# Kernel optimization log

Hardware: AMD Instinct MI355X
Metric: run time of the kernel (lower is better)

The kernel has to match this reference:

```python
import jax, jax.numpy as jnp
import numpy as np

N, E = 50000, 800000
IN_DIM, HEADS, OUT_DIM = 128, 4, 32
NEG_SLOPE = 0.2
EPS = 1e-16


def setup_inputs() -> dict:
    key = jax.random.key(0)
    k = jax.random.split(key, 6)
    x = jax.random.normal(k[0], (N, IN_DIM), dtype=jnp.float32)
    edge_index = jax.random.randint(k[1], (2, E), 0, N, dtype=jnp.int64)
    # xavier-uniform-ish params
    lim_w = float(np.sqrt(6.0 / (IN_DIM + HEADS * OUT_DIM)))
    W = jax.random.uniform(k[2], (HEADS * OUT_DIM, IN_DIM), minval=-lim_w, maxval=lim_w, dtype=jnp.float32)
    lim_a = float(np.sqrt(6.0 / (1 + HEADS * OUT_DIM)))
    att_src = jax.random.uniform(k[3], (1, HEADS, OUT_DIM), minval=-lim_a, maxval=lim_a, dtype=jnp.float32)
    att_dst = jax.random.uniform(k[4], (1, HEADS, OUT_DIM), minval=-lim_a, maxval=lim_a, dtype=jnp.float32)
    bias = jnp.zeros((HEADS * OUT_DIM,), dtype=jnp.float32)
    return {"x": x, "edge_index": edge_index, "W": W, "att_src": att_src, "att_dst": att_dst, "bias": bias}


def reference(x, edge_index, W, att_src, att_dst, bias):
    n = x.shape[0]
    h = (x @ W.T).reshape(n, HEADS, OUT_DIM)           # (N,H,D)
    src, dst = edge_index[0], edge_index[1]
    a_src = jnp.sum(h * att_src, axis=-1)              # (N,H)
    a_dst = jnp.sum(h * att_dst, axis=-1)              # (N,H)
    alpha = a_src[src] + a_dst[dst]                    # (E,H)
    alpha = jax.nn.leaky_relu(alpha, NEG_SLOPE)
    # segment (per-dst) softmax over edges, per head
    m = jax.ops.segment_max(alpha, dst, num_segments=n)   # (N,H)
    ex = jnp.exp(alpha - m[dst])
    s = jax.ops.segment_sum(ex, dst, num_segments=n)      # (N,H)
    alpha = ex / (s[dst] + EPS)                            # (E,H)
    # dropout p=0 (eval) -> identity
    msg = h[src] * alpha[..., None]                        # (E,H,D)
    out = jax.ops.segment_sum(msg, dst, num_segments=n)    # (N,H,D)
    out = out.reshape(n, HEADS * OUT_DIM) + bias
    alpha_pooled = alpha.mean(axis=-1)                     # (E,)
    return out, alpha_pooled
```

## Files before the change

kernel.cpp:

```cpp
#include <hip/hip_runtime.h>

#define NNODES 50000
#define NEDGES 800000
#define HD 128
#define NEG 0.2f
#define MTILE 64
#define LDW 136
#define MAXD 64
#define GEMMB ((NNODES + MTILE - 1) / MTILE)
#define NBINS 196
#define CAP 5120
#define ABLK ((NEDGES + 2047) / 2048)

typedef __attribute__((ext_vector_type(8))) short short8;
typedef __attribute__((ext_vector_type(4))) float floatx4;

static __device__ inline unsigned short f2bf(float f) {
    unsigned u = __float_as_uint(f);
    return (unsigned short)((u + 0x7FFF + ((u >> 16) & 1)) >> 16);
}
static __device__ inline float bf2f(unsigned short u) {
    return __uint_as_float(((unsigned)u) << 16);
}
static __device__ inline float lrelu_exp(float a) {
    a = (a > 0.f) ? a : NEG * a;
    return __expf(a);
}

__global__ __launch_bounds__(256, 4) void gat_main(
    const float* __restrict__ x, const float* __restrict__ W,
    const float* __restrict__ att_src, const float* __restrict__ att_dst,
    const int* __restrict__ ei,
    unsigned short* __restrict__ h, float* __restrict__ asrc,
    float* __restrict__ adst, int* __restrict__ Sg, int* __restrict__ sbuf)
{
    __shared__ __align__(16) unsigned short Wl[128 * LDW];
    const int t = threadIdx.x;

    if (blockIdx.x >= GEMMB) {
        int* hist = (int*)Wl;
        int* sh   = hist + 256;
        int* run  = sh + 256;
        int* lbuf = run + 256;
        const int blk = blockIdx.x - GEMMB;
        const int e0 = blk * 2048 + t * 8;
        const bool act = (e0 < NEDGES);
        const int cnt = (blk == ABLK - 1) ? (NEDGES - blk * 2048) : 2048;
        int4 s0 = make_int4(0, 0, 0, 0), s1 = s0, d0 = s0, d1 = s0;
        if (act) {
            s0 = *(const int4*)(ei + e0);
            s1 = *(const int4*)(ei + e0 + 4);
            d0 = *(const int4*)(ei + NEDGES + e0);
            d1 = *(const int4*)(ei + NEDGES + e0 + 4);
        }
        hist[t] = 0;
        __syncthreads();
        if (act) {
            atomicAdd(&hist[d0.x >> 8], 1); atomicAdd(&hist[d0.y >> 8], 1);
            atomicAdd(&hist[d0.z >> 8], 1); atomicAdd(&hist[d0.w >> 8], 1);
            atomicAdd(&hist[d1.x >> 8], 1); atomicAdd(&hist[d1.y >> 8], 1);
            atomicAdd(&hist[d1.z >> 8], 1); atomicAdd(&hist[d1.w >> 8], 1);
        }
        __syncthreads();
        int hv = hist[t];
        sh[t] = hv;
        __syncthreads();
        for (int off = 1; off < 256; off <<= 1) {
            int u = (t >= off) ? sh[t - off] : 0;
            __syncthreads();
            sh[t] += u;
            __syncthreads();
        }
        int ex = sh[t] - hv;
        run[t] = ex;
        Sg[blk * 257 + t] = ex;
        if (t == 0) Sg[blk * 257 + 256] = cnt;
        __syncthreads();
        if (act) {
            int ss[8] = {s0.x, s0.y, s0.z, s0.w, s1.x, s1.y, s1.z, s1.w};
            int dd[8] = {d0.x, d0.y, d0.z, d0.w, d1.x, d1.y, d1.z, d1.w};
#pragma unroll
            for (int j = 0; j < 8; j++) {
                int slot = atomicAdd(&run[dd[j] >> 8], 1);
                lbuf[slot] = ((dd[j] & 255) << 16) | ss[j];
            }
        }
        __syncthreads();
        for (int i = t; i < cnt; i += 256)
            sbuf[blk * 2048 + i] = lbuf[i];
        return;
    }

    const int rowBase = blockIdx.x * MTILE;

    for (int idx = t * 8; idx < 128 * 128; idx += 2048) {
        int r = idx >> 7, c = idx & 127;
        float4 v0 = *(const float4*)(W + idx);
        float4 v1 = *(const float4*)(W + idx + 4);
        short8 u;
        u[0] = (short)f2bf(v0.x); u[1] = (short)f2bf(v0.y);
        u[2] = (short)f2bf(v0.z); u[3] = (short)f2bf(v0.w);
        u[4] = (short)f2bf(v1.x); u[5] = (short)f2bf(v1.y);
        u[6] = (short)f2bf(v1.z); u[7] = (short)f2bf(v1.w);
        *(short8*)(Wl + r * LDW + c) = u;
    }

    const int wave = t >> 6;
    const int lane = t & 63;
    const int c16  = lane & 15;
    const int quad = lane >> 4;
    const int xr   = rowBase + wave * 16 + c16;
    short8 av[4];
#pragma unroll
    for (int kc = 0; kc < 4; kc++) {
        float4 v0 = make_float4(0.f, 0.f, 0.f, 0.f);
        float4 v1 = v0;
        if (xr < NNODES) {
            const float* p = x + (size_t)xr * 128 + kc * 32 + quad * 8;
            v0 = *(const float4*)p;
            v1 = *(const float4*)(p + 4);
        }
        short8 u;
        u[0] = (short)f2bf(v0.x); u[1] = (short)f2bf(v0.y);
        u[2] = (short)f2bf(v0.z); u[3] = (short)f2bf(v0.w);
        u[4] = (short)f2bf(v1.x); u[5] = (short)f2bf(v1.y);
        u[6] = (short)f2bf(v1.z); u[7] = (short)f2bf(v1.w);
        av[kc] = u;
    }
    __syncthreads();

    floatx4 acc[8];
#pragma unroll
    for (int nt = 0; nt < 8; nt++) acc[nt] = (floatx4)(0.f);

#pragma unroll
    for (int kc = 0; kc < 4; kc++) {
#pragma unroll
        for (int nt = 0; nt < 8; nt++) {
            short8 bv = *(const short8*)(Wl + (nt * 16 + c16) * LDW + kc * 32 + quad * 8);
            acc[nt] = __builtin_amdgcn_mfma_f32_16x16x32_bf16(av[kc], bv, acc[nt], 0, 0, 0);
        }
    }

    float As[8], Ad[8];
#pragma unroll
    for (int nt = 0; nt < 8; nt++) {
        As[nt] = att_src[nt * 16 + c16];
        Ad[nt] = att_dst[nt * 16 + c16];
    }
#pragma unroll
    for (int r = 0; r < 4; r++) {
        const int gr = rowBase + wave * 16 + quad * 4 + r;
#pragma unroll
        for (int hh = 0; hh < 4; hh++) {
            float ps = acc[2 * hh][r] * As[2 * hh] + acc[2 * hh + 1][r] * As[2 * hh + 1];
            float pd = acc[2 * hh][r] * Ad[2 * hh] + acc[2 * hh + 1][r] * Ad[2 * hh + 1];
#pragma unroll
            for (int m = 8; m >= 1; m >>= 1) {
                ps += __shfl_xor(ps, m, 64);
                pd += __shfl_xor(pd, m, 64);
            }
            if (c16 == 0 && gr < NNODES) {
                asrc[gr * 4 + hh] = ps;
                adst[gr * 4 + hh] = pd;
            }
        }
    }

    __syncthreads();
#pragma unroll
    for (int r = 0; r < 4; r++) {
        const int lr = wave * 16 + quad * 4 + r;
#pragma unroll
        for (int nt = 0; nt < 8; nt++)
            Wl[lr * LDW + nt * 16 + c16] = f2bf(acc[nt][r]);
    }
    __syncthreads();
    for (int idx = t * 8; idx < MTILE * 128; idx += 2048) {
        int r = idx >> 7, c = idx & 127;
        int g = rowBase + r;
        if (g < NNODES)
            *(short8*)(h + (size_t)g * HD + c) = *(const short8*)(Wl + r * LDW + c);
    }
}

__global__ __launch_bounds__(1024) void gat_bin(
    const int* __restrict__ Sg, const int* __restrict__ sbuf,
    const float* __restrict__ asrc, const float* __restrict__ adst,
    int* __restrict__ coffB, int* __restrict__ coffE,
    unsigned short* __restrict__ csr, float* __restrict__ rsumr)
{
    __shared__ int s0arr[391];
    __shared__ int segoff[391];
    __shared__ int ebi[CAP];
    __shared__ unsigned short ebs[CAP];
    __shared__ int hist[256], run[256], sh[512];
    const int t = threadIdx.x;
    const int b = blockIdx.x;

    int s0v = 0, lenv = 0;
    if (t < 391) {
        s0v = Sg[t * 257 + b];
        lenv = Sg[t * 257 + b + 1] - s0v;
        s0arr[t] = s0v;
    }
    if (t < 256) hist[t] = 0;
    if (t < 512) sh[t] = (t < 391) ? lenv : 0;
    __syncthreads();
    for (int off = 1; off < 512; off <<= 1) {
        int u = (t < 512 && t >= off) ? sh[t - off] : 0;
        __syncthreads();
        if (t < 512) sh[t] += u;
        __syncthreads();
    }
    if (t < 391) segoff[t] = sh[t] - lenv;
    __syncthreads();
    const int c_b = sh[390];

    for (int i = t; i < c_b; i += 1024) {
        int lo = 0, hi = 390;
        while (lo < hi) {
            int mid = (lo + hi + 1) >> 1;
            if (segoff[mid] <= i) lo = mid; else hi = mid - 1;
        }
        int e = sbuf[lo * 2048 + s0arr[lo] + (i - segoff[lo])];
        ebi[i] = e;
        atomicAdd(&hist[(e >> 16) & 255], 1);
    }
    __syncthreads();

    int hv = (t < 256) ? hist[t] : 0;
    int ex = 0;
    if (t < 256) sh[t] = hv;
    __syncthreads();
    for (int off = 1; off < 256; off <<= 1) {
        int u = (t < 256 && t >= off) ? sh[t - off] : 0;
        __syncthreads();
        if (t < 256) sh[t] += u;
        __syncthreads();
    }
    if (t < 256) {
        ex = sh[t] - hv;
        run[t] = ex;
        int n = b * 256 + t;
        if (n < NNODES) {
            coffB[n] = b * CAP + ex;
            coffE[n] = b * CAP + ex + hv;
        }
    }
    __syncthreads();

    for (int i = t; i < c_b; i += 1024) {
        int e = ebi[i];
        int slot = atomicAdd(&run[(e >> 16) & 255], 1);
        ebs[slot] = (unsigned short)(e & 0xFFFF);
    }
    __syncthreads();

    for (int i = t; i < c_b; i += 1024)
        csr[(size_t)b * CAP + i] = ebs[i];

    if (t < 256) {
        int n = b * 256 + t;
        if (n < NNODES) {
            const float4 bn = *(const float4*)(adst + n * 4);
            float4 s4 = make_float4(0.f, 0.f, 0.f, 0.f);
            for (int i = ex; i < ex + hv; i++) {
                int s = ebs[i];
                float4 a = *(const float4*)(asrc + s * 4);
                s4.x += lrelu_exp(a.x + bn.x);
                s4.y += lrelu_exp(a.y + bn.y);
                s4.z += lrelu_exp(a.z + bn.z);
                s4.w += lrelu_exp(a.w + bn.w);
            }
            float4 r4;
            r4.x = 1.f / (s4.x + 1e-16f);
            r4.y = 1.f / (s4.y + 1e-16f);
            r4.z = 1.f / (s4.z + 1e-16f);
            r4.w = 1.f / (s4.w + 1e-16f);
            *(float4*)(rsumr + n * 4) = r4;
        }
    }
}

__global__ __launch_bounds__(256) void gat_node(
    const int* __restrict__ coffB, const int* __restrict__ coffE,
    const unsigned short* __restrict__ csr,
    const float* __restrict__ asrc, const float* __restrict__ adst,
    const unsigned short* __restrict__ h, const float* __restrict__ bias,
    float* __restrict__ out, const float* __restrict__ rsumr)
{
    __shared__ unsigned short sh_src[4 * MAXD];
    __shared__ float sh_w[4 * MAXD * 4];
    const int t = threadIdx.x;
    const int w = t >> 6;
    const int lane = t & 63;
    const int n = blockIdx.x * 4 + w;
    const int beg = coffB[n], end = coffE[n];
    const int deg = end - beg;
    const int lim = (deg < MAXD) ? deg : MAXD;
    const int base = w * MAXD;

    const float4 rs4 = *(const float4*)(rsumr + n * 4);

    if (lane < lim) {
        int s = csr[beg + lane];
        const float4 bn = *(const float4*)(adst + n * 4);
        float4 a = *(const float4*)(asrc + s * 4);
        float4 wv;
        wv.x = lrelu_exp(a.x + bn.x);
        wv.y = lrelu_exp(a.y + bn.y);
        wv.z = lrelu_exp(a.z + bn.z);
        wv.w = lrelu_exp(a.w + bn.w);
        sh_src[base + lane] = (unsigned short)s;
        *(float4*)(sh_w + (base + lane) * 4) = wv;
    }

    const int quad = lane >> 4;
    const int i16  = lane & 15;
    const int head = i16 >> 2;
    const float rsel = (head == 0) ? rs4.x : (head == 1) ? rs4.y
                      : (head == 2) ? rs4.z : rs4.w;

    float accA[8], accB[8];
#pragma unroll
    for (int m = 0; m < 8; m++) { accA[m] = 0.f; accB[m] = 0.f; }

    int j = 0;
    for (; j + 16 <= lim; j += 16) {
        int e0 = j + quad, e1 = j + 4 + quad, e2 = j + 8 + quad, e3 = j + 12 + quad;
        int s0 = sh_src[base + e0];
        int s1 = sh_src[base + e1];
        int s2 = sh_src[base + e2];
        int s3 = sh_src[base + e3];
        float w0 = sh_w[(base + e0) * 4 + head] * rsel;
        float w1 = sh_w[(base + e1) * 4 + head] * rsel;
        float w2 = sh_w[(base + e2) * 4 + head] * rsel;
        float w3 = sh_w[(base + e3) * 4 + head] * rsel;
        short8 u0 = *(const short8*)(h + (size_t)s0 * HD + i16 * 8);
        short8 u1 = *(const short8*)(h + (size_t)s1 * HD + i16 * 8);
        short8 u2 = *(const short8*)(h + (size_t)s2 * HD + i16 * 8);
        short8 u3 = *(const short8*)(h + (size_t)s3 * HD + i16 * 8);
#pragma unroll
        for (int m = 0; m < 8; m++) {
            accA[m] = fmaf(bf2f((unsigned short)u0[m]), w0, accA[m]);
            accB[m] = fmaf(bf2f((unsigned short)u1[m]), w1, accB[m]);
            accA[m] = fmaf(bf2f((unsigned short)u2[m]), w2, accA[m]);
            accB[m] = fmaf(bf2f((unsigned short)u3[m]), w3, accB[m]);
        }
    }
    for (; j + 4 <= lim; j += 4) {
        int e0 = j + quad;
        int s0 = sh_src[base + e0];
        float w0 = sh_w[(base + e0) * 4 + head] * rsel;
        short8 u0 = *(const short8*)(h + (size_t)s0 * HD + i16 * 8);
#pragma unroll
        for (int m = 0; m < 8; m++)
            accA[m] = fmaf(bf2f((unsigned short)u0[m]), w0, accA[m]);
    }
    if (quad < lim - j) {
        int s0 = sh_src[base + j + quad];
        float w0 = sh_w[(base + j + quad) * 4 + head] * rsel;
        short8 u0 = *(const short8*)(h + (size_t)s0 * HD + i16 * 8);
#pragma unroll
        for (int m = 0; m < 8; m++)
            accA[m] = fmaf(bf2f((unsigned short)u0[m]), w0, accA[m]);
    }
    if (deg > MAXD) {
        const float4 bn = *(const float4*)(adst + n * 4);
        const float bnh = (head == 0) ? bn.x : (head == 1) ? bn.y
                         : (head == 2) ? bn.z : bn.w;
        for (int jj = beg + MAXD + quad; jj < end; jj += 4) {
            int s0 = csr[jj];
            float w0 = lrelu_exp(asrc[s0 * 4 + head] + bnh) * rsel;
            short8 u0 = *(const short8*)(h + (size_t)s0 * HD + i16 * 8);
#pragma unroll
            for (int m = 0; m < 8; m++)
                accA[m] = fmaf(bf2f((unsigned short)u0[m]), w0, accA[m]);
        }
    }

#pragma unroll
    for (int m = 0; m < 8; m++) {
        accA[m] += accB[m];
        accA[m] += __shfl_xor(accA[m], 16, 64);
        accA[m] += __shfl_xor(accA[m], 32, 64);
    }
    if (quad < 2) {
        const float4 b4 = *(const float4*)(bias + i16 * 8 + quad * 4);
        float4 st;
        if (quad == 0) {
            st.x = accA[0] + b4.x; st.y = accA[1] + b4.y;
            st.z = accA[2] + b4.z; st.w = accA[3] + b4.w;
        } else {
            st.x = accA[4] + b4.x; st.y = accA[5] + b4.y;
            st.z = accA[6] + b4.z; st.w = accA[7] + b4.w;
        }
        *(float4*)(out + (size_t)n * HD + i16 * 8 + quad * 4) = st;
    }
}

static __device__ inline float apool1(
    int s, int d, const float* __restrict__ asrc,
    const float* __restrict__ adst, const float* __restrict__ rsumr)
{
    float4 a = *(const float4*)(asrc + s * 4);
    float4 b = *(const float4*)(adst + d * 4);
    float4 r = *(const float4*)(rsumr + d * 4);
    return 0.25f * (lrelu_exp(a.x + b.x) * r.x + lrelu_exp(a.y + b.y) * r.y +
                    lrelu_exp(a.z + b.z) * r.z + lrelu_exp(a.w + b.w) * r.w);
}

__global__ __launch_bounds__(256) void gat_apool(
    const int* __restrict__ ei, const float* __restrict__ asrc,
    const float* __restrict__ adst, const float* __restrict__ rsumr,
    float* __restrict__ apool)
{
    int e0 = (blockIdx.x * 256 + threadIdx.x) * 4;
    if (e0 >= NEDGES) return;
    int4 s = *(const int4*)(ei + e0);
    int4 d = *(const int4*)(ei + NEDGES + e0);
    float4 r;
    r.x = apool1(s.x, d.x, asrc, adst, rsumr);
    r.y = apool1(s.y, d.y, asrc, adst, rsumr);
    r.z = apool1(s.z, d.z, asrc, adst, rsumr);
    r.w = apool1(s.w, d.w, asrc, adst, rsumr);
    *(float4*)(apool + e0) = r;
}

extern "C" void kernel_launch(void* const* d_in, const int* in_sizes, int n_in,
                              void* d_out, int out_size, void* d_ws, size_t ws_size,
                              hipStream_t stream)
{
    const float* x       = (const float*)d_in[0];
    const int*   ei      = (const int*)d_in[1];
    const float* W       = (const float*)d_in[2];
    const float* att_src = (const float*)d_in[3];
    const float* att_dst = (const float*)d_in[4];
    const float* bias    = (const float*)d_in[5];

    float* out   = (float*)d_out;
    float* apool = out + (size_t)NNODES * HD;

    unsigned short* h = (unsigned short*)d_ws;
    float* asrc  = (float*)(h + (size_t)NNODES * HD);
    float* adst  = asrc + NNODES * 4;
    float* rsumr = adst + NNODES * 4;
    int*   Sg    = (int*)(rsumr + NNODES * 4);
    int*   coffB = Sg + ABLK * 257 + 4;
    int*   coffE = coffB + NNODES + 4;
    int*   sbuf  = coffE + NNODES + 4;
    unsigned short* csr = (unsigned short*)(sbuf + (size_t)ABLK * 2048);

    gat_main<<<GEMMB + ABLK, 256, 0, stream>>>(
        x, W, att_src, att_dst, ei, h, asrc, adst, Sg, sbuf);
    gat_bin<<<NBINS, 1024, 0, stream>>>(
        Sg, sbuf, asrc, adst, coffB, coffE, csr, rsumr);
    gat_node<<<NNODES / 4, 256, 0, stream>>>(
        coffB, coffE, csr, asrc, adst, h, bias, out, rsumr);
    gat_apool<<<(NEDGES / 4 + 255) / 256, 256, 0, stream>>>(
        ei, asrc, adst, rsumr, apool);
}
```

Baseline: 166.5 us.

## Parallelize softmax denominators with LDS atomics and fuse apool into node kernel

The per-destination exp-sum in the binning kernel is computed by all 1024 threads, each handling edges with shared-memory float atomics, instead of one thread per node looping serially over its edges. The edge-pooling kernel is merged into the node aggregation kernel as extra leading blocks, removing a launch and allowing overlap. The node kernel also gets a higher occupancy hint. This trades the serial loop's load imbalance for LDS atomic contention and nondeterministic summation order.

Result: slower. 172.4 us (+3.5%).

```diff
diff --git a/kernel.cpp b/kernel.cpp
--- a/kernel.cpp
+++ b/kernel.cpp
@@ -11,6 +11,7 @@
 #define NBINS 196
 #define CAP 5120
 #define ABLK ((NEDGES + 2047) / 2048)
+#define APOOLB ((NEDGES / 4 + 255) / 256)
 
 typedef __attribute__((ext_vector_type(8))) short short8;
 typedef __attribute__((ext_vector_type(4))) float floatx4;
@@ -195,6 +196,7 @@
     __shared__ int ebi[CAP];
     __shared__ unsigned short ebs[CAP];
     __shared__ int hist[256], run[256], sh[512];
+    __shared__ float sum4[256 * 4];
     const int t = threadIdx.x;
     const int b = blockIdx.x;
 
@@ -205,6 +207,7 @@
         s0arr[t] = s0v;
     }
     if (t < 256) hist[t] = 0;
+    sum4[t] = 0.f;
     if (t < 512) sh[t] = (t < 391) ? lenv : 0;
     __syncthreads();
     for (int off = 1; off < 512; off <<= 1) {
@@ -230,7 +233,6 @@
     __syncthreads();
 
     int hv = (t < 256) ? hist[t] : 0;
-    int ex = 0;
     if (t < 256) sh[t] = hv;
     __syncthreads();
     for (int off = 1; off < 256; off <<= 1) {
@@ -240,7 +242,7 @@
         __syncthreads();
     }
     if (t < 256) {
-        ex = sh[t] - hv;
+        int ex = sh[t] - hv;
         run[t] = ex;
         int n = b * 256 + t;
         if (n < NNODES) {
@@ -259,43 +261,72 @@
 
     for (int i = t; i < c_b; i += 1024)
         csr[(size_t)b * CAP + i] = ebs[i];
+    for (int i = t; i < c_b; i += 1024) {
+        int e = ebi[i];
+        int f = (e >> 16) & 255;
+        int s = e & 0xFFFF;
+        float4 a  = *(const float4*)(asrc + s * 4);
+        float4 bn = *(const float4*)(adst + (b * 256 + f) * 4);
+        atomicAdd(&sum4[f * 4 + 0], lrelu_exp(a.x + bn.x));
+        atomicAdd(&sum4[f * 4 + 1], lrelu_exp(a.y + bn.y));
+        atomicAdd(&sum4[f * 4 + 2], lrelu_exp(a.z + bn.z));
+        atomicAdd(&sum4[f * 4 + 3], lrelu_exp(a.w + bn.w));
+    }
+    __syncthreads();
 
     if (t < 256) {
         int n = b * 256 + t;
         if (n < NNODES) {
-            const float4 bn = *(const float4*)(adst + n * 4);
-            float4 s4 = make_float4(0.f, 0.f, 0.f, 0.f);
-            for (int i = ex; i < ex + hv; i++) {
-                int s = ebs[i];
-                float4 a = *(const float4*)(asrc + s * 4);
-                s4.x += lrelu_exp(a.x + bn.x);
-                s4.y += lrelu_exp(a.y + bn.y);
-                s4.z += lrelu_exp(a.z + bn.z);
-                s4.w += lrelu_exp(a.w + bn.w);
-            }
             float4 r4;
-            r4.x = 1.f / (s4.x + 1e-16f);
-            r4.y = 1.f / (s4.y + 1e-16f);
-            r4.z = 1.f / (s4.z + 1e-16f);
-            r4.w = 1.f / (s4.w + 1e-16f);
+            r4.x = 1.f / (sum4[t * 4 + 0] + 1e-16f);
+            r4.y = 1.f / (sum4[t * 4 + 1] + 1e-16f);
+            r4.z = 1.f / (sum4[t * 4 + 2] + 1e-16f);
+            r4.w = 1.f / (sum4[t * 4 + 3] + 1e-16f);
             *(float4*)(rsumr + n * 4) = r4;
         }
     }
 }
 
-__global__ __launch_bounds__(256) void gat_node(
+static __device__ inline float apool1(
+    int s, int d, const float* __restrict__ asrc,
+    const float* __restrict__ adst, const float* __restrict__ rsumr)
+{
+    float4 a = *(const float4*)(asrc + s * 4);
+    float4 b = *(const float4*)(adst + d * 4);
+    float4 r = *(const float4*)(rsumr + d * 4);
+    return 0.25f * (lrelu_exp(a.x + b.x) * r.x + lrelu_exp(a.y + b.y) * r.y +
+                    lrelu_exp(a.z + b.z) * r.z + lrelu_exp(a.w + b.w) * r.w);
+}
+
+__global__ __launch_bounds__(256, 8) void gat_node(
     const int* __restrict__ coffB, const int* __restrict__ coffE,
     const unsigned short* __restrict__ csr,
     const float* __restrict__ asrc, const float* __restrict__ adst,
     const unsigned short* __restrict__ h, const float* __restrict__ bias,
-    float* __restrict__ out, const float* __restrict__ rsumr)
+    float* __restrict__ out, const float* __restrict__ rsumr,
+    const int* __restrict__ ei, float* __restrict__ apool)
 {
     __shared__ unsigned short sh_src[4 * MAXD];
     __shared__ float sh_w[4 * MAXD * 4];
     const int t = threadIdx.x;
+
+    if (blockIdx.x < APOOLB) {
+        int e0 = (blockIdx.x * 256 + t) * 4;
+        if (e0 >= NEDGES) return;
+        int4 s = *(const int4*)(ei + e0);
+        int4 d = *(const int4*)(ei + NEDGES + e0);
+        float4 r;
+        r.x = apool1(s.x, d.x, asrc, adst, rsumr);
+        r.y = apool1(s.y, d.y, asrc, adst, rsumr);
+        r.z = apool1(s.z, d.z, asrc, adst, rsumr);
+        r.w = apool1(s.w, d.w, asrc, adst, rsumr);
+        *(float4*)(apool + e0) = r;
+        return;
+    }
+
     const int w = t >> 6;
     const int lane = t & 63;
-    const int n = blockIdx.x * 4 + w;
+    const int n = (blockIdx.x - APOOLB) * 4 + w;
     const int beg = coffB[n], end = coffE[n];
     const int deg = end - beg;
     const int lim = (deg < MAXD) ? deg : MAXD;
@@ -400,34 +431,6 @@
     }
 }
 
-static __device__ inline float apool1(
-    int s, int d, const float* __restrict__ asrc,
-    const float* __restrict__ adst, const float* __restrict__ rsumr)
-{
-    float4 a = *(const float4*)(asrc + s * 4);
-    float4 b = *(const float4*)(adst + d * 4);
-    float4 r = *(const float4*)(rsumr + d * 4);
-    return 0.25f * (lrelu_exp(a.x + b.x) * r.x + lrelu_exp(a.y + b.y) * r.y +
-                    lrelu_exp(a.z + b.z) * r.z + lrelu_exp(a.w + b.w) * r.w);
-}
-
-__global__ __launch_bounds__(256) void gat_apool(
-    const int* __restrict__ ei, const float* __restrict__ asrc,
-    const float* __restrict__ adst, const float* __restrict__ rsumr,
-    float* __restrict__ apool)
-{
-    int e0 = (blockIdx.x * 256 + threadIdx.x) * 4;
-    if (e0 >= NEDGES) return;
-    int4 s = *(const int4*)(ei + e0);
-    int4 d = *(const int4*)(ei + NEDGES + e0);
-    float4 r;
-    r.x = apool1(s.x, d.x, asrc, adst, rsumr);
-    r.y = apool1(s.y, d.y, asrc, adst, rsumr);
-    r.z = apool1(s.z, d.z, asrc, adst, rsumr);
-    r.w = apool1(s.w, d.w, asrc, adst, rsumr);
-    *(float4*)(apool + e0) = r;
-}
-
 extern "C" void kernel_launch(void* const* d_in, const int* in_sizes, int n_in,
                               void* d_out, int out_size, void* d_ws, size_t ws_size,
                               hipStream_t stream)
@@ -456,8 +459,6 @@
         x, W, att_src, att_dst, ei, h, asrc, adst, Sg, sbuf);
     gat_bin<<<NBINS, 1024, 0, stream>>>(
         Sg, sbuf, asrc, adst, coffB, coffE, csr, rsumr);
-    gat_node<<<NNODES / 4, 256, 0, stream>>>(
-        coffB, coffE, csr, asrc, adst, h, bias, out, rsumr);
-    gat_apool<<<(NEDGES / 4 + 255) / 256, 256, 0, stream>>>(
-        ei, asrc, adst, rsumr, apool);
-}
+    gat_node<<<APOOLB + NNODES / 4, 256, 0, stream>>>(
+        coffB, coffE, csr, asrc, adst, h, bias, out, rsumr, ei, apool);
+}
```
